# Kernel optimization log

Hardware: AMD Instinct MI355X
Metric: run time of the kernel (lower is better)

The kernel has to match this reference:

```python
import jax, jax.numpy as jnp
import numpy as np

STRIDE = 1
PADDING = 1

def setup_inputs() -> dict:
    key = jax.random.key(0)
    k1, k2, k3 = jax.random.split(key, 3)
    N, C_in, H, W = 32, 128, 56, 56
    C_out, K = 256, 3
    inputs = jax.random.normal(k1, (N, C_in, H, W), dtype=jnp.float32)
    # trunc_normal(std=0.1) approximated by clipped normal
    filters = jnp.clip(jax.random.normal(k2, (C_out, C_in, K, K), dtype=jnp.float32) * 0.1, -0.2, 0.2)
    bias = jnp.clip(jax.random.normal(k3, (C_out,), dtype=jnp.float32) * 0.1, -0.2, 0.2)
    return {"inputs": inputs, "filters": filters, "bias": bias}

def reference(inputs, filters, bias):
    # Equivalent of the quadruple-loop conv: standard cross-correlation,
    # NCHW input, OIHW filters, stride/padding from module config.
    out = jax.lax.conv_general_dilated(
        inputs, filters,
        window_strides=(STRIDE, STRIDE),
        padding=[(PADDING, PADDING), (PADDING, PADDING)],
        dimension_numbers=("NCHW", "OIHW", "NCHW"),
    )
    out = out + bias[None, :, None, None]
    return out
```

## Files before the change

kernel.cpp:

```cpp
#include <hip/hip_runtime.h>

#define CIN    128
#define HH     56
#define WW_    56
#define NBATCH 32
#define COUT   256
#define KTOT   1152
#define PLANE  3136
#define HP     58
#define BM     128
#define BN     128
#define BK     64
#define NXROWS (NBATCH * HP)

#define WB_OFF   0
#define XP_OFF   (1u << 20)

typedef __attribute__((ext_vector_type(8))) short bf16x8;
typedef __attribute__((ext_vector_type(4))) float f32x4;

__device__ __forceinline__ unsigned short f2bf(float f) {
    unsigned int u = __builtin_bit_cast(unsigned int, f);
    u += 0x7fffu + ((u >> 16) & 1u);
    return (unsigned short)(u >> 16);
}

__device__ __forceinline__ void gl_lds16(const void* g, void* l) {
    __builtin_amdgcn_global_load_lds(
        (const __attribute__((address_space(1))) void*)g,
        (__attribute__((address_space(3))) void*)l, 16, 0, 0);
}

__global__ __launch_bounds__(256)
void prep(const float* __restrict__ in, const float* __restrict__ w,
          unsigned short* __restrict__ xp, unsigned short* __restrict__ wb) {
    __shared__ __align__(16) unsigned short Lx[16 * 456];
    __shared__ __align__(16) unsigned short Lw[KTOT];

    const int b = blockIdx.x;
    const int t = threadIdx.x;

    if (b >= NXROWS) {
        const int o = b - NXROWS;
        const float4* src = (const float4*)(w + (size_t)o * KTOT);
        #pragma unroll
        for (int e = 0; e < 2; ++e) {
            const int q = t + e * 256;
            if (q < 288) {
                const float4 v = src[q];
                #pragma unroll
                for (int u = 0; u < 4; ++u) {
                    const int idx = q * 4 + u;
                    const int ci  = idx / 9;
                    const int tap = idx - ci * 9;
                    Lw[tap * 128 + ci] = f2bf(((const float*)&v)[u]);
                }
            }
        }
        __syncthreads();
        if (t < 144)
            ((uint4*)(wb + (size_t)o * KTOT))[t] = ((const uint4*)Lw)[t];
        return;
    }

    const int n  = b / HP;
    const int ho = b - n * HP;
    uint4* orow = (uint4*)(xp + (((size_t)n * HP + ho) * HP) * CIN);

    if (ho == 0 || ho == HP - 1) {
        #pragma unroll
        for (int e = 0; e < 4; ++e) {
            const int idx = t + e * 256;
            if (idx < 928) orow[idx] = (uint4){0u, 0u, 0u, 0u};
        }
        return;
    }

    const int h = ho - 1;
    {
        const int ci = t >> 1;
        const int w0 = (t & 1) * 28;
        const float4* ib = (const float4*)(in + ((size_t)n * CIN + ci) * PLANE
                                              + (size_t)h * WW_ + w0);
        unsigned short* Lp = &Lx[(ci >> 3) * 456 + w0 * 8 + (ci & 7)];
        #pragma unroll
        for (int q = 0; q < 7; ++q) {
            const float4 v = ib[q];
            Lp[(q * 4 + 0) * 8] = f2bf(v.x);
            Lp[(q * 4 + 1) * 8] = f2bf(v.y);
            Lp[(q * 4 + 2) * 8] = f2bf(v.z);
            Lp[(q * 4 + 3) * 8] = f2bf(v.w);
        }
    }
    __syncthreads();

    #pragma unroll
    for (int e = 0; e < 4; ++e) {
        const int idx = t + e * 256;
        if (idx < 928) {
            const int wo = idx >> 4;
            const int ch = idx & 15;
            uint4 pk = (uint4){0u, 0u, 0u, 0u};
            if (wo >= 1 && wo <= WW_)
                pk = *(const uint4*)&Lx[ch * 456 + (wo - 1) * 8];
            orow[idx] = pk;
        }
    }
}

__global__ __launch_bounds__(256, 2)
void conv_mfma(const unsigned short* __restrict__ wb,
               const unsigned short* __restrict__ xp,
               const float* __restrict__ bias,
               float* __restrict__ out)
{
    __shared__ __align__(16) unsigned short Asm_[BM * BK];
    __shared__ __align__(16) unsigned short Bsm_[BN * BK];

    const int t    = threadIdx.x;
    const int pix0 = blockIdx.x * BN;
    const int c0   = blockIdx.y * BM;

    const int slot = t & 7;
    const int r32  = t >> 3;
    const int swiz = (slot ^ (r32 & 7)) * 16;

    const char* aBase = (const char*)wb + (size_t)(c0 + r32) * (KTOT * 2) + swiz;
    const char* bBase[4];
    #pragma unroll
    for (int p = 0; p < 4; ++p) {
        const int pix = pix0 + r32 + p * 32;
        const int n   = pix / PLANE;
        const int rem = pix - n * PLANE;
        const int h   = rem / WW_;
        const int w   = rem - h * WW_;
        bBase[p] = (const char*)xp + ((size_t)(n * HP + h) * HP + w) * (CIN * 2) + swiz;
    }

    const int lane = t & 63;
    const int wave = t >> 6;
    const int wm   = (wave & 1) * 64;
    const int wn   = (wave >> 1) * 64;
    const int lr   = lane & 15;
    const int quad = lane >> 4;
    const int rmod = lr & 7;

    f32x4 acc[4][4];
    #pragma unroll
    for (int i = 0; i < 4; ++i)
        #pragma unroll
        for (int j = 0; j < 4; ++j)
            acc[i][j] = (f32x4){0.f, 0.f, 0.f, 0.f};

    char* const asmb = (char*)Asm_;
    char* const bsmb = (char*)Bsm_;

    for (int tap = 0; tap < 9; ++tap) {
        const int toff = ((tap / 3) * HP + (tap % 3)) * (CIN * 2);
        for (int ci0b = 0; ci0b < 256; ci0b += 128) {
            const int abyte = tap * 256 + ci0b;
            #pragma unroll
            for (int p = 0; p < 4; ++p)
                gl_lds16(aBase + (size_t)p * 32 * (KTOT * 2) + abyte, asmb + p * 4096 + t * 16);
            #pragma unroll
            for (int p = 0; p < 4; ++p)
                gl_lds16(bBase[p] + toff + ci0b, bsmb + p * 4096 + t * 16);
            __syncthreads();

            #pragma unroll
            for (int kk = 0; kk < 2; ++kk) {
                bf16x8 af[4], bfr[4];
                #pragma unroll
                for (int i = 0; i < 4; ++i) {
                    const int r = wm + i * 16 + lr;
                    const int phys = ((kk * 4 + quad) ^ rmod) * 16;
                    af[i] = *(const bf16x8*)(asmb + r * 128 + phys);
                }
                #pragma unroll
                for (int j = 0; j < 4; ++j) {
                    const int r = wn + j * 16 + lr;
                    const int phys = ((kk * 4 + quad) ^ rmod) * 16;
                    bfr[j] = *(const bf16x8*)(bsmb + r * 128 + phys);
                }
                #pragma unroll
                for (int i = 0; i < 4; ++i)
                    #pragma unroll
                    for (int j = 0; j < 4; ++j)
                        acc[i][j] = __builtin_amdgcn_mfma_f32_16x16x32_bf16(af[i], bfr[j], acc[i][j], 0, 0, 0);
            }
            __syncthreads();
        }
    }

    #pragma unroll
    for (int j = 0; j < 4; ++j) {
        const int pg    = pix0 + wn + j * 16 + lr;
        const int ni    = pg / PLANE;
        const int inner = pg - ni * PLANE;
        float* op = out + (size_t)ni * (COUT * PLANE) + inner;
        #pragma unroll
        for (int i = 0; i < 4; ++i) {
            const int crow = c0 + wm + i * 16 + quad * 4;
            #pragma unroll
            for (int r = 0; r < 4; ++r)
                op[(size_t)(crow + r) * PLANE] = acc[i][j][r] + bias[crow + r];
        }
    }
}

extern "C" void kernel_launch(void* const* d_in, const int* in_sizes, int n_in,
                              void* d_out, int out_size, void* d_ws, size_t ws_size,
                              hipStream_t stream) {
    const float* in   = (const float*)d_in[0];
    const float* wt   = (const float*)d_in[1];
    const float* bias = (const float*)d_in[2];
    float* out        = (float*)d_out;

    unsigned short* wb = (unsigned short*)((char*)d_ws + WB_OFF);
    unsigned short* xp = (unsigned short*)((char*)d_ws + XP_OFF);

    prep<<<NXROWS + COUT, 256, 0, stream>>>(in, wt, xp, wb);

    dim3 grid((NBATCH * PLANE) / BN, COUT / BM);
    conv_mfma<<<grid, 256, 0, stream>>>(wb, xp, bias, out);
}
```

Baseline: 203.3 us.

## Halve K-tile to 32 and raise occupancy to four blocks per CU

The K step per iteration drops from 64 to 32 bf16 elements, which halves shared memory per block (16KB), and launch bounds now request four blocks per CU instead of two. The LDS layout packs two rows per 128-byte line with a new XOR swizzle, and the global-to-LDS load mapping and fragment offsets are recomputed to match. The aim is more resident waves to hide load latency. In exchange the main loop runs 36 iterations with two barriers each instead of 18, so synchronization overhead doubles relative to the MFMA work per step.

Measured after the change: 219.1 us. 7.8% more time.

```diff
diff --git a/kernel.cpp b/kernel.cpp
--- a/kernel.cpp
+++ b/kernel.cpp
@@ -10,7 +10,8 @@
 #define HP     58
 #define BM     128
 #define BN     128
-#define BK     64
+#define BKS    32
+#define NSTEP  36
 #define NXROWS (NBATCH * HP)
 
 #define WB_OFF   0
@@ -108,33 +109,35 @@
     }
 }
 
-__global__ __launch_bounds__(256, 2)
+__global__ __launch_bounds__(256, 4)
 void conv_mfma(const unsigned short* __restrict__ wb,
                const unsigned short* __restrict__ xp,
                const float* __restrict__ bias,
                float* __restrict__ out)
 {
-    __shared__ __align__(16) unsigned short Asm_[BM * BK];
-    __shared__ __align__(16) unsigned short Bsm_[BN * BK];
+    __shared__ __align__(16) unsigned short Asm_[BM * BKS];
+    __shared__ __align__(16) unsigned short Bsm_[BN * BKS];
 
     const int t    = threadIdx.x;
     const int pix0 = blockIdx.x * BN;
     const int c0   = blockIdx.y * BM;
 
-    const int slot = t & 7;
-    const int r32  = t >> 3;
-    const int swiz = (slot ^ (r32 & 7)) * 16;
-
-    const char* aBase = (const char*)wb + (size_t)(c0 + r32) * (KTOT * 2) + swiz;
-    const char* bBase[4];
-    #pragma unroll
-    for (int p = 0; p < 4; ++p) {
-        const int pix = pix0 + r32 + p * 32;
+    const char* aS[2]; const char* bS[2]; int dst[2];
+    #pragma unroll
+    for (int e = 0; e < 2; ++e) {
+        const int u    = t + e * 256;
+        const int line = u >> 3;
+        const int us   = (u & 7) ^ (line & 7);
+        const int row  = 2 * line + (us >> 2);
+        const int ch   = us & 3;
+        aS[e] = (const char*)wb + (size_t)(c0 + row) * (KTOT * 2) + ch * 16;
+        const int pix = pix0 + row;
         const int n   = pix / PLANE;
         const int rem = pix - n * PLANE;
         const int h   = rem / WW_;
         const int w   = rem - h * WW_;
-        bBase[p] = (const char*)xp + ((size_t)(n * HP + h) * HP + w) * (CIN * 2) + swiz;
+        bS[e] = (const char*)xp + ((size_t)(n * HP + h) * HP + w) * (CIN * 2) + ch * 16;
+        dst[e] = u * 16;
     }
 
     const int lane = t & 63;
@@ -143,7 +146,15 @@
     const int wn   = (wave >> 1) * 64;
     const int lr   = lane & 15;
     const int quad = lane >> 4;
-    const int rmod = lr & 7;
+
+    int offA[4], offB[4];
+    #pragma unroll
+    for (int i = 0; i < 4; ++i) {
+        const int ra = wm + i * 16 + lr;
+        offA[i] = (ra >> 1) * 128 + ((((ra & 1) * 4 + quad) ^ ((ra >> 1) & 7)) * 16);
+        const int rb = wn + i * 16 + lr;
+        offB[i] = (rb >> 1) * 128 + ((((rb & 1) * 4 + quad) ^ ((rb >> 1) & 7)) * 16);
+    }
 
     f32x4 acc[4][4];
     #pragma unroll
@@ -155,41 +166,27 @@
     char* const asmb = (char*)Asm_;
     char* const bsmb = (char*)Bsm_;
 
-    for (int tap = 0; tap < 9; ++tap) {
-        const int toff = ((tap / 3) * HP + (tap % 3)) * (CIN * 2);
-        for (int ci0b = 0; ci0b < 256; ci0b += 128) {
-            const int abyte = tap * 256 + ci0b;
+    for (int hi = 0; hi < NSTEP; ++hi) {
+        const int tap  = hi >> 2;
+        const int aoff = hi * 64;
+        const int boff = ((tap / 3) * HP + (tap % 3)) * (CIN * 2) + (hi & 3) * 64;
+        gl_lds16(aS[0] + aoff, asmb + dst[0]);
+        gl_lds16(aS[1] + aoff, asmb + dst[1]);
+        gl_lds16(bS[0] + boff, bsmb + dst[0]);
+        gl_lds16(bS[1] + boff, bsmb + dst[1]);
+        __syncthreads();
+
+        bf16x8 af[4], bfr[4];
+        #pragma unroll
+        for (int i = 0; i < 4; ++i) af[i]  = *(const bf16x8*)(asmb + offA[i]);
+        #pragma unroll
+        for (int j = 0; j < 4; ++j) bfr[j] = *(const bf16x8*)(bsmb + offB[j]);
+        #pragma unroll
+        for (int i = 0; i < 4; ++i)
             #pragma unroll
-            for (int p = 0; p < 4; ++p)
-                gl_lds16(aBase + (size_t)p * 32 * (KTOT * 2) + abyte, asmb + p * 4096 + t * 16);
-            #pragma unroll
-            for (int p = 0; p < 4; ++p)
-                gl_lds16(bBase[p] + toff + ci0b, bsmb + p * 4096 + t * 16);
-            __syncthreads();
-
-            #pragma unroll
-            for (int kk = 0; kk < 2; ++kk) {
-                bf16x8 af[4], bfr[4];
-                #pragma unroll
-                for (int i = 0; i < 4; ++i) {
-                    const int r = wm + i * 16 + lr;
-                    const int phys = ((kk * 4 + quad) ^ rmod) * 16;
-                    af[i] = *(const bf16x8*)(asmb + r * 128 + phys);
-                }
-                #pragma unroll
-                for (int j = 0; j < 4; ++j) {
-                    const int r = wn + j * 16 + lr;
-                    const int phys = ((kk * 4 + quad) ^ rmod) * 16;
-                    bfr[j] = *(const bf16x8*)(bsmb + r * 128 + phys);
-                }
-                #pragma unroll
-                for (int i = 0; i < 4; ++i)
-                    #pragma unroll
-                    for (int j = 0; j < 4; ++j)
-                        acc[i][j] = __builtin_amdgcn_mfma_f32_16x16x32_bf16(af[i], bfr[j], acc[i][j], 0, 0, 0);
-            }
-            __syncthreads();
-        }
+            for (int j = 0; j < 4; ++j)
+                acc[i][j] = __builtin_amdgcn_mfma_f32_16x16x32_bf16(af[i], bfr[j], acc[i][j], 0, 0, 0);
+        __syncthreads();
     }
 
     #pragma unroll
```
